# Kernel tuning notes

Hardware: AMD Instinct MI355X
Metric: run time of the kernel (lower is better)

Reference implementation:

```python
import jax, jax.numpy as jnp
import numpy as np

B, T, D, H, DH = 8, 1024, 512, 8, 64
DEPTH, V, FF = 8, 6400, 2048
NH, BS = 8, 64            # n_hashes, bucket_size
NB = T // BS              # 16 buckets
SELF_ATTN_VALUE = -5e4


def setup_inputs() -> dict:
    key = jax.random.key(0)
    ks = jax.random.split(key, 12)
    def n(k, shape, s=0.02):
        return jax.random.normal(k, shape, dtype=jnp.float32) * s
    return {
        "input_ids": jax.random.randint(ks[0], (B, T), 0, V),
        "token_emb": n(ks[1], (V, D)),
        "pos_emb": n(ks[2], (T, D)),
        "ln_attn_g": jnp.ones((DEPTH, D), jnp.float32),
        "ln_attn_b": jnp.zeros((DEPTH, D), jnp.float32),
        "Wqk": n(ks[3], (DEPTH, D, D)),
        "Wv": n(ks[4], (DEPTH, D, D)),
        "Wo": n(ks[5], (DEPTH, D, D)),
        "ln_ff_g": jnp.ones((DEPTH, D), jnp.float32),
        "ln_ff_b": jnp.zeros((DEPTH, D), jnp.float32),
        "W1": n(ks[6], (DEPTH, D, FF)),
        "b1": jnp.zeros((DEPTH, FF), jnp.float32),
        "W2": n(ks[7], (DEPTH, FF, D)),
        "b2": jnp.zeros((DEPTH, D), jnp.float32),
        "ln_f_g": jnp.ones((D,), jnp.float32),
        "ln_f_b": jnp.zeros((D,), jnp.float32),
        "Wfc": n(ks[8], (D, D)),
        # fixed random LSH rotation matrices, one per layer: [depth, dim_head, n_hashes, n_buckets//2]
        "rotations": jax.random.normal(ks[9], (DEPTH, DH, NH, NB // 2), dtype=jnp.float32),
    }


def layer_norm(x, g, b):
    m = jnp.mean(x, -1, keepdims=True)
    v = jnp.mean(jnp.square(x - m), -1, keepdims=True)
    return (x - m) * jax.lax.rsqrt(v + 1e-5) * g + b


def lsh_attention(x, Wqk, Wv, Wo, rot):
    """Reformer LSH self-attention: shared QK, NH hash rounds, bucket sort,
    chunked attention with 1-chunk look-back, multi-round logsumexp combine."""
    Bx = x.shape[0]
    qk = (x @ Wqk).reshape(Bx, T, H, DH).transpose(0, 2, 1, 3).reshape(Bx * H, T, DH)
    v = (x @ Wv).reshape(Bx, T, H, DH).transpose(0, 2, 1, 3).reshape(Bx * H, T, DH)

    # --- hashing: argmax over [rotated, -rotated] -> bucket ids per round ---
    rotated = jnp.einsum('btd,dhr->bhtr', qk, rot)                       # [BH,NH,T,NB/2]
    buckets = jnp.argmax(jnp.concatenate([rotated, -rotated], -1), -1)   # [BH,NH,T]
    buckets = buckets + (jnp.arange(NH) * NB)[None, :, None]
    buckets = buckets.reshape(Bx * H, NH * T)

    # --- stable sort by (bucket, position) ---
    ticker = jnp.arange(NH * T)
    b_t = buckets * T + (ticker % T)[None, :]
    sticker = jnp.argsort(b_t, axis=-1)
    undo = jnp.argsort(sticker, axis=-1)
    st = sticker % T                                                     # original positions
    sqk = jnp.take_along_axis(qk, st[..., None], axis=1)                 # [BH,NH*T,DH]
    sv = jnp.take_along_axis(v, st[..., None], axis=1)

    # --- chunk: NH*NB chunks of length BS, keys look back one chunk ---
    nc = NH * NB
    bq_t = st.reshape(-1, nc, BS)
    bq = sqk.reshape(-1, nc, BS, DH)
    bk = bq / (jnp.linalg.norm(bq, axis=-1, keepdims=True) + 1e-8)       # unit-length keys
    bv = sv.reshape(-1, nc, BS, DH)

    def look_back(t):
        return jnp.concatenate([t, jnp.roll(t, 1, axis=1)], axis=2)

    bk, bv, bkv_t = look_back(bk), look_back(bv), look_back(bq_t)

    dots = jnp.einsum('bnqd,bnkd->bnqk', bq, bk) * (DH ** -0.5)          # [BH,nc,BS,2BS]
    self_mask = bq_t[..., :, None] == bkv_t[..., None, :]
    dots = jnp.where(self_mask, SELF_ATTN_VALUE, dots)

    logits = jax.nn.logsumexp(dots, axis=-1, keepdims=True)
    probs = jnp.exp(dots - logits)
    bo = jnp.einsum('bnqk,bnkd->bnqd', probs, bv)

    # --- unsort and combine hash rounds weighted by per-round logsumexp ---
    so = bo.reshape(-1, NH * T, DH)
    slog = logits.reshape(-1, NH * T)
    o = jnp.take_along_axis(so, undo[..., None], axis=1).reshape(-1, NH, T, DH)
    lg = jnp.take_along_axis(slog, undo, axis=1).reshape(-1, NH, T, 1)
    w = jax.nn.softmax(lg, axis=1)
    out = jnp.sum(o * w, axis=1)                                         # [BH,T,DH]
    out = out.reshape(Bx, H, T, DH).transpose(0, 2, 1, 3).reshape(Bx, T, D)
    return out @ Wo


def reference(input_ids, token_emb, pos_emb, ln_attn_g, ln_attn_b, Wqk, Wv, Wo,
              ln_ff_g, ln_ff_b, W1, b1, W2, b2, ln_f_g, ln_f_b, Wfc, rotations):
    x = token_emb[input_ids] + pos_emb[None, :, :]
    # reversible residual streams: y1 = x1 + attn(norm(x2)); y2 = x2 + ff(norm(y1))
    x1, x2 = x, x
    for l in range(DEPTH):
        x1 = x1 + lsh_attention(layer_norm(x2, ln_attn_g[l], ln_attn_b[l]),
                                Wqk[l], Wv[l], Wo[l], rotations[l])
        h = layer_norm(x1, ln_ff_g[l], ln_ff_b[l])
        x2 = x2 + (jax.nn.gelu(h @ W1[l] + b1[l]) @ W2[l] + b2[l])
    x = 0.5 * (x1 + x2)
    x = layer_norm(x, ln_f_g, ln_f_b)
    return jnp.mean(x, axis=1) @ Wfc                                     # [B, embedding_dim]
```

## Files before the change

kernel.cpp:

```cpp
#include <hip/hip_runtime.h>
#include <hip/hip_bf16.h>
#include <cstdint>
#include <cstddef>

#define B_ 8
#define T_ 1024
#define D_ 512
#define H_ 8
#define DH_ 64
#define DEPTH_ 8
#define FF_ 2048
#define NH_ 8
#define BS_ 64
#define NB_ 16
#define NC_ 128
#define BH_ 64
#define ROWS_ 8192

typedef __attribute__((ext_vector_type(8))) short bf16x8;
typedef __attribute__((ext_vector_type(4))) float f32x4;

typedef __attribute__((address_space(1))) const unsigned int g_u32;
typedef __attribute__((address_space(3))) unsigned int l_u32;
__device__ __forceinline__ void gload16(const void* g, void* l) {
  __builtin_amdgcn_global_load_lds((g_u32*)g, (l_u32*)l, 16, 0, 0);
}

__device__ __forceinline__ float wave_sum(float v) {
#pragma unroll
  for (int o = 1; o < 64; o <<= 1) v += __shfl_xor(v, o);
  return v;
}

__device__ __forceinline__ float gelu_f(float u) {
  float c = u + 0.044715f * u * u * u;
  float t = tanhf(0.7978845608028654f * c);
  return 0.5f * u * (1.0f + t);
}

__global__ __launch_bounds__(128) void k_embed(const int* __restrict__ ids,
                                               const float* __restrict__ te,
                                               const float* __restrict__ pe,
                                               float* __restrict__ x1,
                                               float* __restrict__ x2) {
  int bt = blockIdx.x;
  int t = bt & (T_ - 1);
  int d = threadIdx.x * 4;
  int id = ids[bt];
  float4 v = *(const float4*)(te + (size_t)id * D_ + d);
  float4 p = *(const float4*)(pe + (size_t)t * D_ + d);
  v.x += p.x; v.y += p.y; v.z += p.z; v.w += p.w;
  *(float4*)(x1 + (size_t)bt * D_ + d) = v;
  *(float4*)(x2 + (size_t)bt * D_ + d) = v;
}

__global__ __launch_bounds__(256) void k_wt(const float* __restrict__ W,
                                            __hip_bfloat16* __restrict__ WT,
                                            int K, int N) {
  const float* Wl = W + (size_t)blockIdx.z * K * N;
  __hip_bfloat16* WTl = WT + (size_t)blockIdx.z * K * N;
  __shared__ float tile[32][33];
  int n0 = blockIdx.x * 32, k0 = blockIdx.y * 32;
  int tx = threadIdx.x & 31, ty = threadIdx.x >> 5;
#pragma unroll
  for (int i = 0; i < 32; i += 8)
    tile[ty + i][tx] = Wl[(size_t)(k0 + ty + i) * N + n0 + tx];
  __syncthreads();
#pragma unroll
  for (int i = 0; i < 32; i += 8)
    WTl[(size_t)(n0 + ty + i) * K + k0 + tx] = __float2bfloat16(tile[tx][ty + i]);
}

__global__ __launch_bounds__(256) void k_ln(const float* __restrict__ x,
                                            const float* __restrict__ xb,
                                            const float* __restrict__ g,
                                            const float* __restrict__ bb,
                                            float* __restrict__ y,
                                            __hip_bfloat16* __restrict__ yb) {
  int w = threadIdx.x >> 6, lane = threadIdx.x & 63;
  size_t row = (size_t)blockIdx.x * 4 + w;
  const float* xr = x + row * D_ + lane * 8;
  float v[8];
  *(float4*)(v)     = *(const float4*)(xr);
  *(float4*)(v + 4) = *(const float4*)(xr + 4);
  if (xb) {
    const float* x2r = xb + row * D_ + lane * 8;
    float u[8];
    *(float4*)(u)     = *(const float4*)(x2r);
    *(float4*)(u + 4) = *(const float4*)(x2r + 4);
#pragma unroll
    for (int i = 0; i < 8; ++i) v[i] = 0.5f * (v[i] + u[i]);
  }
  float s = 0.f;
#pragma unroll
  for (int i = 0; i < 8; ++i) s += v[i];
  s = wave_sum(s);
  float m = s * (1.0f / D_);
  float q = 0.f;
#pragma unroll
  for (int i = 0; i < 8; ++i) { float d = v[i] - m; q += d * d; }
  q = wave_sum(q);
  float inv = 1.0f / sqrtf(q * (1.0f / D_) + 1e-5f);
  float gg[8], bv[8];
  *(float4*)(gg)     = *(const float4*)(g + lane * 8);
  *(float4*)(gg + 4) = *(const float4*)(g + lane * 8 + 4);
  *(float4*)(bv)     = *(const float4*)(bb + lane * 8);
  *(float4*)(bv + 4) = *(const float4*)(bb + lane * 8 + 4);
  float o[8];
#pragma unroll
  for (int i = 0; i < 8; ++i) o[i] = (v[i] - m) * inv * gg[i] + bv[i];
  if (y) {
    float* yr = y + row * D_ + lane * 8;
    *(float4*)(yr)     = *(float4*)(o);
    *(float4*)(yr + 4) = *(float4*)(o + 4);
  }
  if (yb) {
    __hip_bfloat16 o16[8];
#pragma unroll
    for (int i = 0; i < 8; ++i) o16[i] = __float2bfloat16(o[i]);
    *(uint4*)(yb + row * D_ + lane * 8) = *(uint4*)o16;
  }
}

__global__ __launch_bounds__(256) void k_sgemm(const float* __restrict__ A,
                                               const float* __restrict__ Bm,
                                               float* __restrict__ C,
                                               int N, int K) {
  __shared__ float As[32][128];
  __shared__ float Bs[32][128];
  const int bn0 = blockIdx.x * 128;
  const int bm0 = blockIdx.y * 128;
  const int tid = threadIdx.x;
  const int w = tid >> 6, lane = tid & 63;
  const int wy = w >> 1, wx = w & 1;
  const int ly = lane >> 3, lx = lane & 7;
  const int rm = wy * 64 + ly * 8;
  const int cn = wx * 64 + lx * 8;
  float acc[8][8] = {};

  for (int k0 = 0; k0 < K; k0 += 32) {
#pragma unroll
    for (int ld = 0; ld < 4; ++ld) {
      int f = tid + ld * 256;
      int ar = f >> 3;
      int ac = (f & 7) << 2;
      float4 av = *(const float4*)(A + (size_t)(bm0 + ar) * K + k0 + ac);
      As[ac + 0][ar] = av.x; As[ac + 1][ar] = av.y;
      As[ac + 2][ar] = av.z; As[ac + 3][ar] = av.w;
      int br = f >> 5;
      int bc = (f & 31) << 2;
      *(float4*)(&Bs[br][bc]) = *(const float4*)(Bm + (size_t)(k0 + br) * N + bn0 + bc);
    }
    __syncthreads();
#pragma unroll
    for (int kk = 0; kk < 32; ++kk) {
      float a[8], b[8];
      *(float4*)(a)     = *(const float4*)(&As[kk][rm]);
      *(float4*)(a + 4) = *(const float4*)(&As[kk][rm + 4]);
      *(float4*)(b)     = *(const float4*)(&Bs[kk][cn]);
      *(float4*)(b + 4) = *(const float4*)(&Bs[kk][cn + 4]);
#pragma unroll
      for (int i = 0; i < 8; ++i)
#pragma unroll
        for (int j = 0; j < 8; ++j) acc[i][j] += a[i] * b[j];
    }
    __syncthreads();
  }
#pragma unroll
  for (int i = 0; i < 8; ++i) {
    float* crow = C + (size_t)(bm0 + rm + i) * N + bn0 + cn;
#pragma unroll
    for (int j0 = 0; j0 < 8; j0 += 4)
      *(float4*)(crow + j0) = make_float4(acc[i][j0], acc[i][j0 + 1], acc[i][j0 + 2], acc[i][j0 + 3]);
  }
}

template <int EPI>
__global__ __launch_bounds__(256) void k_bgemm(const __hip_bfloat16* __restrict__ A,
                                               const __hip_bfloat16* __restrict__ BT,
                                               const float* __restrict__ bias,
                                               void* __restrict__ Cv,
                                               int N, int K) {
  __shared__ __align__(16) __hip_bfloat16 As[128 * 32];
  __shared__ __align__(16) __hip_bfloat16 Bs[128 * 32];
  const int bn0 = blockIdx.x * 128;
  const int bm0 = blockIdx.y * 128;
  const int tid = threadIdx.x;
  const int w = tid >> 6, lane = tid & 63;
  const int wy = w >> 1, wx = w & 1;
  const int g = lane >> 4, lr = lane & 15;
  f32x4 acc[4][4] = {};

  const __hip_bfloat16* Abase = A + (size_t)bm0 * K;
  const __hip_bfloat16* Bbase = BT + (size_t)bn0 * K;

  for (int k0 = 0; k0 < K; k0 += 32) {
#pragma unroll
    for (int it = 0; it < 2; ++it) {
      int f = it * 256 + w * 64 + lane;
      int row = f >> 2;
      int kc = ((f & 3) ^ ((row >> 1) & 3)) << 3;
      gload16(Abase + (size_t)row * K + k0 + kc, &As[(it * 256 + w * 64) * 8]);
      gload16(Bbase + (size_t)row * K + k0 + kc, &Bs[(it * 256 + w * 64) * 8]);
    }
    __syncthreads();
    bf16x8 af[4], bfr[4];
#pragma unroll
    for (int m = 0; m < 4; ++m) {
      int row = wy * 64 + m * 16 + lr;
      af[m] = *(const bf16x8*)(&As[row * 32 + ((g ^ ((row >> 1) & 3)) << 3)]);
    }
#pragma unroll
    for (int n = 0; n < 4; ++n) {
      int row = wx * 64 + n * 16 + lr;
      bfr[n] = *(const bf16x8*)(&Bs[row * 32 + ((g ^ ((row >> 1) & 3)) << 3)]);
    }
#pragma unroll
    for (int m = 0; m < 4; ++m)
#pragma unroll
      for (int n = 0; n < 4; ++n)
        acc[m][n] = __builtin_amdgcn_mfma_f32_16x16x32_bf16(af[m], bfr[n], acc[m][n], 0, 0, 0);
    __syncthreads();
  }

  const int colb = bn0 + wx * 64 + lr;
  const int rowb = bm0 + wy * 64 + (g << 2);
#pragma unroll
  for (int m = 0; m < 4; ++m) {
#pragma unroll
    for (int n = 0; n < 4; ++n) {
      int c = colb + n * 16;
      int r0 = rowb + m * 16;
      float bsv = (EPI == 2 || EPI == 3) ? bias[c] : 0.f;
#pragma unroll
      for (int j = 0; j < 4; ++j) {
        float vlu = acc[m][n][j] + bsv;
        size_t idx = (size_t)(r0 + j) * N + c;
        if (EPI == 0) ((float*)Cv)[idx] = vlu;
        else if (EPI == 1) ((float*)Cv)[idx] += vlu;
        else if (EPI == 2) ((__hip_bfloat16*)Cv)[idx] = __float2bfloat16(gelu_f(vlu));
        else ((float*)Cv)[idx] += vlu;
      }
    }
  }
}

__global__ __launch_bounds__(128) void k_bucket(const float* __restrict__ qk,
                                                const float* __restrict__ rotL,
                                                unsigned char* __restrict__ bkt) {
  int blk = blockIdx.x;
  int tc = blk & 7, h = (blk >> 3) & 7, b = blk >> 6;
  int t0 = tc << 7;
  __shared__ float qs[128][65];
  __shared__ float rs[4096];
  int tid = threadIdx.x;
  for (int f = tid; f < 4096; f += 128) rs[f] = rotL[f];
  const float* base = qk + ((size_t)(b * T_ + t0)) * D_ + h * DH_;
  for (int f = tid; f < 2048; f += 128) {
    int rw = f >> 4, c4 = (f & 15) << 2;
    float4 v = *(const float4*)(base + (size_t)rw * D_ + c4);
    qs[rw][c4] = v.x; qs[rw][c4 + 1] = v.y; qs[rw][c4 + 2] = v.z; qs[rw][c4 + 3] = v.w;
  }
  __syncthreads();
  float s[64];
#pragma unroll
  for (int jr = 0; jr < 64; ++jr) s[jr] = 0.f;
  for (int d = 0; d < 64; ++d) {
    float q = qs[tid][d];
    const float* rp = rs + d * 64;
#pragma unroll
    for (int j4 = 0; j4 < 16; ++j4) {
      float4 rv = *(const float4*)(rp + j4 * 4);
      s[j4 * 4 + 0] += q * rv.x; s[j4 * 4 + 1] += q * rv.y;
      s[j4 * 4 + 2] += q * rv.z; s[j4 * 4 + 3] += q * rv.w;
    }
  }
  int bh = b * H_ + h;
#pragma unroll
  for (int r = 0; r < 8; ++r) {
    float best = s[r * 8];
    int bi = 0;
#pragma unroll
    for (int idx = 1; idx < 16; ++idx) {
      float v = (idx < 8) ? s[r * 8 + idx] : -s[r * 8 + idx - 8];
      if (v > best) { best = v; bi = idx; }
    }
    bkt[((size_t)(bh * NH_ + r)) * T_ + t0 + tid] = (unsigned char)bi;
  }
}

__global__ __launch_bounds__(1024) void k_sort(const unsigned char* __restrict__ bkt,
                                               int* __restrict__ st,
                                               int* __restrict__ undo) {
  int r = blockIdx.x & 7, bh = blockIdx.x >> 3;
  int t = threadIdx.x;
  int bk = bkt[((size_t)(bh * NH_ + r)) * T_ + t];
  int w = t >> 6, lane = t & 63;
  __shared__ int cnt[16][16];
  __shared__ int off[16][16];
  __shared__ int tot[16];
  __shared__ int stt[16];
  unsigned long long below = (1ULL << lane) - 1ULL;
  int myrank = 0;
#pragma unroll
  for (int bb = 0; bb < 16; ++bb) {
    unsigned long long m = __ballot(bk == bb);
    if (bk == bb) myrank = __popcll(m & below);
    if (lane == 0) cnt[w][bb] = __popcll(m);
  }
  __syncthreads();
  if (t < 16) {
    int run = 0;
    for (int ww = 0; ww < 16; ++ww) { off[ww][t] = run; run += cnt[ww][t]; }
    tot[t] = run;
  }
  __syncthreads();
  if (t == 0) {
    int run = 0;
    for (int bb = 0; bb < 16; ++bb) { stt[bb] = run; run += tot[bb]; }
  }
  __syncthreads();
  int pos = stt[bk] + off[w][bk] + myrank;
  st[((size_t)(bh * NH_ + r)) * T_ + pos] = t;
  undo[((size_t)(bh * NH_ + r)) * T_ + t] = pos;
}

__global__ __launch_bounds__(256) void k_attn(const float* __restrict__ qk,
                                              const float* __restrict__ vv,
                                              const int* __restrict__ st,
                                              __hip_bfloat16* __restrict__ ob,
                                              float* __restrict__ lgb) {
  __shared__ __align__(16) __hip_bfloat16 Kb[128 * 72];
  __shared__ __align__(16) __hip_bfloat16 VbT[64 * 136];
  __shared__ __align__(16) __hip_bfloat16 PbQb[64 * 136];
  __shared__ int pos[128];

  const int c = blockIdx.x, bh = blockIdx.y;
  const int b = bh >> 3, h = bh & 7;
  const int r = c >> 4;
  const int pc = (c + NC_ - 1) & (NC_ - 1);
  const int tid = threadIdx.x;

  if (tid < 128) {
    int sc = (tid < 64) ? c : pc;
    int slot = ((sc & 15) << 6) + (tid & 63);
    pos[tid] = st[((size_t)(bh * NH_ + (sc >> 4))) * T_ + slot];
  }
  __syncthreads();

  const float* qkbase = qk + ((size_t)b * T_) * D_ + h * DH_;
  const float* vbase  = vv + ((size_t)b * T_) * D_ + h * DH_;

#pragma unroll
  for (int ld = 0; ld < 8; ++ld) {
    int f = ld * 256 + tid;
    int rw = f >> 4, c4 = (f & 15) << 2;
    float4 v = *(const float4*)(qkbase + (size_t)pos[rw] * D_ + c4);
    float ss = v.x * v.x + v.y * v.y + v.z * v.z + v.w * v.w;
    ss += __shfl_xor(ss, 1); ss += __shfl_xor(ss, 2);
    ss += __shfl_xor(ss, 4); ss += __shfl_xor(ss, 8);
    float inv = 1.0f / (sqrtf(ss) + 1e-8f);
    __hip_bfloat16 kb4[4];
    kb4[0] = __float2bfloat16(v.x * inv); kb4[1] = __float2bfloat16(v.y * inv);
    kb4[2] = __float2bfloat16(v.z * inv); kb4[3] = __float2bfloat16(v.w * inv);
    *(uint2*)(&Kb[rw * 72 + c4]) = *(uint2*)kb4;
  }
#pragma unroll
  for (int ld = 0; ld < 4; ++ld) {
    int f = ld * 256 + tid;
    int rw = f >> 4, c4 = (f & 15) << 2;
    float4 v = *(const float4*)(qkbase + (size_t)pos[rw] * D_ + c4);
    __hip_bfloat16 qb4[4];
    qb4[0] = __float2bfloat16(v.x * 0.125f); qb4[1] = __float2bfloat16(v.y * 0.125f);
    qb4[2] = __float2bfloat16(v.z * 0.125f); qb4[3] = __float2bfloat16(v.w * 0.125f);
    *(uint2*)(&PbQb[rw * 72 + c4]) = *(uint2*)qb4;
  }
#pragma unroll
  for (int ld = 0; ld < 8; ++ld) {
    int f = ld * 256 + tid;
    int rw = f >> 4, c4 = (f & 15) << 2;
    float4 v = *(const float4*)(vbase + (size_t)pos[rw] * D_ + c4);
    VbT[(c4 + 0) * 136 + rw] = __float2bfloat16(v.x);
    VbT[(c4 + 1) * 136 + rw] = __float2bfloat16(v.y);
    VbT[(c4 + 2) * 136 + rw] = __float2bfloat16(v.z);
    VbT[(c4 + 3) * 136 + rw] = __float2bfloat16(v.w);
  }
  __syncthreads();

  const int w = tid >> 6, lane = tid & 63;
  const int g = lane >> 4, l15 = lane & 15;
  const int q0 = w * 16;

  bf16x8 af0 = *(const bf16x8*)(&PbQb[(q0 + l15) * 72 + g * 8]);
  bf16x8 af1 = *(const bf16x8*)(&PbQb[(q0 + l15) * 72 + 32 + g * 8]);
  f32x4 dacc[8];
#pragma unroll
  for (int n = 0; n < 8; ++n) dacc[n] = (f32x4){0.f, 0.f, 0.f, 0.f};
#pragma unroll
  for (int n = 0; n < 8; ++n) {
    bf16x8 b0 = *(const bf16x8*)(&Kb[(n * 16 + l15) * 72 + g * 8]);
    bf16x8 b1 = *(const bf16x8*)(&Kb[(n * 16 + l15) * 72 + 32 + g * 8]);
    dacc[n] = __builtin_amdgcn_mfma_f32_16x16x32_bf16(af0, b0, dacc[n], 0, 0, 0);
    dacc[n] = __builtin_amdgcn_mfma_f32_16x16x32_bf16(af1, b1, dacc[n], 0, 0, 0);
  }
  __syncthreads();

  int qpos[4], kpos[8];
#pragma unroll
  for (int reg = 0; reg < 4; ++reg) qpos[reg] = pos[q0 + g * 4 + reg];
#pragma unroll
  for (int n = 0; n < 8; ++n) kpos[n] = pos[n * 16 + l15];
  float pr[8][4];
  float lgt[4];
#pragma unroll
  for (int reg = 0; reg < 4; ++reg) {
    float mx = -3.0e38f;
#pragma unroll
    for (int n = 0; n < 8; ++n) {
      float dv = dacc[n][reg];
      dv = (kpos[n] == qpos[reg]) ? -5.0e4f : dv;
      pr[n][reg] = dv;
      mx = fmaxf(mx, dv);
    }
    mx = fmaxf(mx, __shfl_xor(mx, 1));
    mx = fmaxf(mx, __shfl_xor(mx, 2));
    mx = fmaxf(mx, __shfl_xor(mx, 4));
    mx = fmaxf(mx, __shfl_xor(mx, 8));
    float s = 0.f;
#pragma unroll
    for (int n = 0; n < 8; ++n) { float e = expf(pr[n][reg] - mx); pr[n][reg] = e; s += e; }
    s += __shfl_xor(s, 1); s += __shfl_xor(s, 2);
    s += __shfl_xor(s, 4); s += __shfl_xor(s, 8);
    lgt[reg] = mx + logf(s);
    float isc = 1.0f / s;
#pragma unroll
    for (int n = 0; n < 8; ++n) pr[n][reg] *= isc;
  }
#pragma unroll
  for (int n = 0; n < 8; ++n)
#pragma unroll
    for (int reg = 0; reg < 4; ++reg)
      PbQb[(q0 + g * 4 + reg) * 136 + n * 16 + l15] = __float2bfloat16(pr[n][reg]);
  const size_t slotbase = ((size_t)(bh * NH_ + r)) * T_ + ((c & 15) << 6);
  if (l15 == 0) {
#pragma unroll
    for (int reg = 0; reg < 4; ++reg)
      lgb[slotbase + q0 + g * 4 + reg] = lgt[reg];
  }
  __syncthreads();

  bf16x8 va[4];
#pragma unroll
  for (int s = 0; s < 4; ++s)
    va[s] = *(const bf16x8*)(&VbT[(w * 16 + l15) * 136 + s * 32 + g * 8]);
#pragma unroll
  for (int n = 0; n < 4; ++n) {
    f32x4 oa = (f32x4){0.f, 0.f, 0.f, 0.f};
#pragma unroll
    for (int s = 0; s < 4; ++s) {
      bf16x8 pb = *(const bf16x8*)(&PbQb[(n * 16 + l15) * 136 + s * 32 + g * 8]);
      oa = __builtin_amdgcn_mfma_f32_16x16x32_bf16(va[s], pb, oa, 0, 0, 0);
    }
    int q = n * 16 + l15;
    int d = w * 16 + g * 4;
    __hip_bfloat16 o4[4];
#pragma unroll
    for (int reg = 0; reg < 4; ++reg) o4[reg] = __float2bfloat16(oa[reg]);
    *(uint2*)(&ob[(slotbase + q) * DH_ + d]) = *(uint2*)o4;
  }
}

__global__ __launch_bounds__(256) void k_combine(const __hip_bfloat16* __restrict__ ob,
                                                 const float* __restrict__ lgb,
                                                 const int* __restrict__ undo,
                                                 __hip_bfloat16* __restrict__ attnb) {
  int g = threadIdx.x >> 6, lane = threadIdx.x & 63;
  int idx = blockIdx.x * 4 + g;
  int bh = idx >> 10, t = idx & (T_ - 1);
  int b = bh >> 3, h = bh & 7;
  int su[8];
  float lg[8];
  float m = -3.0e38f;
#pragma unroll
  for (int r = 0; r < 8; ++r) {
    su[r] = undo[((size_t)(bh * NH_ + r)) * T_ + t];
    lg[r] = lgb[((size_t)(bh * NH_ + r)) * T_ + su[r]];
    m = fmaxf(m, lg[r]);
  }
  float s = 0.f;
#pragma unroll
  for (int r = 0; r < 8; ++r) { lg[r] = expf(lg[r] - m); s += lg[r]; }
  float invs = 1.0f / s;
  float o = 0.f;
#pragma unroll
  for (int r = 0; r < 8; ++r)
    o += lg[r] * invs * __bfloat162float(ob[(((size_t)(bh * NH_ + r)) * T_ + su[r]) * DH_ + lane]);
  attnb[((size_t)(b * T_ + t)) * D_ + h * DH_ + lane] = __float2bfloat16(o);
}

__global__ void k_zero(float* __restrict__ p, int n) {
  int i = blockIdx.x * blockDim.x + threadIdx.x;
  if (i < n) p[i] = 0.f;
}

__global__ __launch_bounds__(256) void k_colsum(const float* __restrict__ xn,
                                                float* __restrict__ mean) {
  int b = blockIdx.x, dc = blockIdx.y, tc = blockIdx.z;
  int d = dc * 256 + threadIdx.x;
  float s = 0.f;
  for (int tt = 0; tt < 64; ++tt) {
    int t = tc * 64 + tt;
    s += xn[((size_t)(b * T_ + t)) * D_ + d];
  }
  atomicAdd(&mean[b * D_ + d], s);
}

__global__ __launch_bounds__(512) void k_fc(const float* __restrict__ mean,
                                            const float* __restrict__ Wfc,
                                            float* __restrict__ out) {
  int b = blockIdx.x, n = threadIdx.x;
  __shared__ float ms[512];
  ms[n] = mean[b * D_ + n] * (1.0f / 1024.0f);
  __syncthreads();
  float acc = 0.f;
  for (int d = 0; d < 512; ++d) acc += ms[d] * Wfc[(size_t)d * D_ + n];
  out[b * D_ + n] = acc;
}

extern "C" void kernel_launch(void* const* d_in, const int* in_sizes, int n_in,
                              void* d_out, int out_size, void* d_ws, size_t ws_size,
                              hipStream_t stream) {
  (void)in_sizes; (void)n_in; (void)out_size; (void)ws_size;
  const int*   ids  = (const int*)d_in[0];
  const float* te   = (const float*)d_in[1];
  const float* pe   = (const float*)d_in[2];
  const float* lag  = (const float*)d_in[3];
  const float* lab  = (const float*)d_in[4];
  const float* Wqk  = (const float*)d_in[5];
  const float* Wv   = (const float*)d_in[6];
  const float* Wo   = (const float*)d_in[7];
  const float* lfg  = (const float*)d_in[8];
  const float* lfb  = (const float*)d_in[9];
  const float* W1   = (const float*)d_in[10];
  const float* b1   = (const float*)d_in[11];
  const float* W2   = (const float*)d_in[12];
  const float* b2   = (const float*)d_in[13];
  const float* lnfg = (const float*)d_in[14];
  const float* lnfb = (const float*)d_in[15];
  const float* Wfc  = (const float*)d_in[16];
  const float* rot  = (const float*)d_in[17];

  char* ws = (char*)d_ws;
  size_t off = 0;
  auto carve = [&](size_t bytes) -> void* {
    void* p = ws + off;
    off += (bytes + 255) & ~(size_t)255;
    return p;
  };
  float* x1    = (float*)carve((size_t)ROWS_ * D_ * 4);
  float* x2    = (float*)carve((size_t)ROWS_ * D_ * 4);
  float* xn    = (float*)carve((size_t)ROWS_ * D_ * 4);
  float* qkb   = (float*)carve((size_t)ROWS_ * D_ * 4);
  float* vvb   = (float*)carve((size_t)ROWS_ * D_ * 4);
  __hip_bfloat16* xnb   = (__hip_bfloat16*)carve((size_t)ROWS_ * D_ * 2);
  __hip_bfloat16* attnb = (__hip_bfloat16*)carve((size_t)ROWS_ * D_ * 2);
  __hip_bfloat16* ob    = (__hip_bfloat16*)carve((size_t)BH_ * NH_ * T_ * DH_ * 2);
  __hip_bfloat16* hid   = ob;
  unsigned char* bkt = (unsigned char*)carve((size_t)BH_ * NH_ * T_);
  int*   stb   = (int*)carve((size_t)BH_ * NH_ * T_ * 4);
  int*   undo  = (int*)carve((size_t)BH_ * NH_ * T_ * 4);
  float* lgb   = (float*)carve((size_t)BH_ * NH_ * T_ * 4);
  float* meanb = (float*)carve((size_t)B_ * D_ * 4);
  __hip_bfloat16* WvT = (__hip_bfloat16*)carve((size_t)DEPTH_ * D_ * D_ * 2);
  __hip_bfloat16* WoT = (__hip_bfloat16*)carve((size_t)DEPTH_ * D_ * D_ * 2);
  __hip_bfloat16* W1T = (__hip_bfloat16*)carve((size_t)DEPTH_ * D_ * FF_ * 2);
  __hip_bfloat16* W2T = (__hip_bfloat16*)carve((size_t)DEPTH_ * FF_ * D_ * 2);

  k_wt<<<dim3(D_ / 32, D_ / 32, DEPTH_), 256, 0, stream>>>(Wv, WvT, D_, D_);
  k_wt<<<dim3(D_ / 32, D_ / 32, DEPTH_), 256, 0, stream>>>(Wo, WoT, D_, D_);
  k_wt<<<dim3(FF_ / 32, D_ / 32, DEPTH_), 256, 0, stream>>>(W1, W1T, D_, FF_);
  k_wt<<<dim3(D_ / 32, FF_ / 32, DEPTH_), 256, 0, stream>>>(W2, W2T, FF_, D_);

  k_embed<<<ROWS_, 128, 0, stream>>>(ids, te, pe, x1, x2);

  for (int l = 0; l < DEPTH_; ++l) {
    const float* wqk = Wqk + (size_t)l * D_ * D_;
    const __hip_bfloat16* wvt = WvT + (size_t)l * D_ * D_;
    const __hip_bfloat16* wot = WoT + (size_t)l * D_ * D_;
    const __hip_bfloat16* w1t = W1T + (size_t)l * D_ * FF_;
    const __hip_bfloat16* w2t = W2T + (size_t)l * FF_ * D_;

    k_ln<<<ROWS_ / 4, 256, 0, stream>>>(x2, nullptr, lag + l * D_, lab + l * D_, xn, xnb);
    k_sgemm<<<dim3(D_ / 128, ROWS_ / 128), 256, 0, stream>>>(xn, wqk, qkb, D_, D_);
    k_bgemm<0><<<dim3(D_ / 128, ROWS_ / 128), 256, 0, stream>>>(xnb, wvt, nullptr, vvb, D_, D_);
    k_bucket<<<512, 128, 0, stream>>>(qkb, rot + (size_t)l * 4096, bkt);
    k_sort<<<512, 1024, 0, stream>>>(bkt, stb, undo);
    k_attn<<<dim3(NC_, BH_), 256, 0, stream>>>(qkb, vvb, stb, ob, lgb);
    k_combine<<<BH_ * T_ / 4, 256, 0, stream>>>(ob, lgb, undo, attnb);
    k_bgemm<1><<<dim3(D_ / 128, ROWS_ / 128), 256, 0, stream>>>(attnb, wot, nullptr, x1, D_, D_);

    k_ln<<<ROWS_ / 4, 256, 0, stream>>>(x1, nullptr, lfg + l * D_, lfb + l * D_, nullptr, xnb);
    k_bgemm<2><<<dim3(FF_ / 128, ROWS_ / 128), 256, 0, stream>>>(xnb, w1t, b1 + l * FF_, hid, FF_, D_);
    k_bgemm<3><<<dim3(D_ / 128, ROWS_ / 128), 256, 0, stream>>>(hid, w2t, b2 + l * D_, x2, D_, FF_);
  }

  k_ln<<<ROWS_ / 4, 256, 0, stream>>>(x1, x2, lnfg, lnfb, xn, nullptr);
  k_zero<<<16, 256, 0, stream>>>(meanb, B_ * D_);
  k_colsum<<<dim3(B_, 2, 16), 256, 0, stream>>>(xn, meanb);
  k_fc<<<B_, 512, 0, stream>>>(meanb, Wfc, (float*)d_out);
}
```

Measured before the change: 3.312 ms.

## Precompute bf16 Q/normalized-K and bf16 V to shrink attention gathers

Adds a per-row prep kernel that writes scaled Q and L2-normalized K as bf16, and makes the V projection emit bf16. The attention kernel then gathers bf16 rows with 16-byte loads instead of fp32 rows, recomputing no norms. V is transposed into shared memory through lane shuffles, with an XOR swizzle to avoid bank conflicts. Softmax and combine switch to fast __expf/__logf. The cost is an extra kernel pass and extra bf16 buffers, plus reduced precision in the exp/log.

Measured after the change: 3.200 ms. 3.4% less time.

```diff
diff --git a/kernel.cpp b/kernel.cpp
--- a/kernel.cpp
+++ b/kernel.cpp
@@ -122,6 +122,30 @@
   }
 }
 
+__global__ __launch_bounds__(256) void k_prep(const float* __restrict__ qkb,
+                                              __hip_bfloat16* __restrict__ qsb,
+                                              __hip_bfloat16* __restrict__ knb) {
+  int w = threadIdx.x >> 6, lane = threadIdx.x & 63;
+  size_t row = (size_t)blockIdx.x * 4 + w;
+  const float* xr = qkb + row * D_ + lane * 8;
+  float v[8];
+  *(float4*)(v)     = *(const float4*)(xr);
+  *(float4*)(v + 4) = *(const float4*)(xr + 4);
+  float ss = 0.f;
+#pragma unroll
+  for (int i = 0; i < 8; ++i) ss += v[i] * v[i];
+  ss += __shfl_xor(ss, 1); ss += __shfl_xor(ss, 2); ss += __shfl_xor(ss, 4);
+  float inv = 1.0f / (sqrtf(ss) + 1e-8f);
+  __hip_bfloat16 qo[8], ko[8];
+#pragma unroll
+  for (int i = 0; i < 8; ++i) {
+    qo[i] = __float2bfloat16(v[i] * 0.125f);
+    ko[i] = __float2bfloat16(v[i] * inv);
+  }
+  *(uint4*)(qsb + row * D_ + lane * 8) = *(uint4*)qo;
+  *(uint4*)(knb + row * D_ + lane * 8) = *(uint4*)ko;
+}
+
 __global__ __launch_bounds__(256) void k_sgemm(const float* __restrict__ A,
                                                const float* __restrict__ Bm,
                                                float* __restrict__ C,
@@ -239,7 +263,8 @@
         if (EPI == 0) ((float*)Cv)[idx] = vlu;
         else if (EPI == 1) ((float*)Cv)[idx] += vlu;
         else if (EPI == 2) ((__hip_bfloat16*)Cv)[idx] = __float2bfloat16(gelu_f(vlu));
-        else ((float*)Cv)[idx] += vlu;
+        else if (EPI == 3) ((float*)Cv)[idx] += vlu;
+        else ((__hip_bfloat16*)Cv)[idx] = __float2bfloat16(vlu);
       }
     }
   }
@@ -325,8 +350,9 @@
   undo[((size_t)(bh * NH_ + r)) * T_ + t] = pos;
 }
 
-__global__ __launch_bounds__(256) void k_attn(const float* __restrict__ qk,
-                                              const float* __restrict__ vv,
+__global__ __launch_bounds__(256) void k_attn(const __hip_bfloat16* __restrict__ qs,
+                                              const __hip_bfloat16* __restrict__ kn,
+                                              const __hip_bfloat16* __restrict__ vv,
                                               const int* __restrict__ st,
                                               __hip_bfloat16* __restrict__ ob,
                                               float* __restrict__ lgb) {
@@ -348,42 +374,54 @@
   }
   __syncthreads();
 
-  const float* qkbase = qk + ((size_t)b * T_) * D_ + h * DH_;
-  const float* vbase  = vv + ((size_t)b * T_) * D_ + h * DH_;
-
-#pragma unroll
-  for (int ld = 0; ld < 8; ++ld) {
-    int f = ld * 256 + tid;
-    int rw = f >> 4, c4 = (f & 15) << 2;
-    float4 v = *(const float4*)(qkbase + (size_t)pos[rw] * D_ + c4);
-    float ss = v.x * v.x + v.y * v.y + v.z * v.z + v.w * v.w;
-    ss += __shfl_xor(ss, 1); ss += __shfl_xor(ss, 2);
-    ss += __shfl_xor(ss, 4); ss += __shfl_xor(ss, 8);
-    float inv = 1.0f / (sqrtf(ss) + 1e-8f);
-    __hip_bfloat16 kb4[4];
-    kb4[0] = __float2bfloat16(v.x * inv); kb4[1] = __float2bfloat16(v.y * inv);
-    kb4[2] = __float2bfloat16(v.z * inv); kb4[3] = __float2bfloat16(v.w * inv);
-    *(uint2*)(&Kb[rw * 72 + c4]) = *(uint2*)kb4;
-  }
+  const __hip_bfloat16* qbase = qs + ((size_t)b * T_) * D_ + h * DH_;
+  const __hip_bfloat16* kbase = kn + ((size_t)b * T_) * D_ + h * DH_;
+  const __hip_bfloat16* vbase = vv + ((size_t)b * T_) * D_ + h * DH_;
+
 #pragma unroll
   for (int ld = 0; ld < 4; ++ld) {
     int f = ld * 256 + tid;
-    int rw = f >> 4, c4 = (f & 15) << 2;
-    float4 v = *(const float4*)(qkbase + (size_t)pos[rw] * D_ + c4);
-    __hip_bfloat16 qb4[4];
-    qb4[0] = __float2bfloat16(v.x * 0.125f); qb4[1] = __float2bfloat16(v.y * 0.125f);
-    qb4[2] = __float2bfloat16(v.z * 0.125f); qb4[3] = __float2bfloat16(v.w * 0.125f);
-    *(uint2*)(&PbQb[rw * 72 + c4]) = *(uint2*)qb4;
-  }
-#pragma unroll
-  for (int ld = 0; ld < 8; ++ld) {
+    int rw = f >> 3, c8 = (f & 7) << 3;
+    *(uint4*)(&Kb[rw * 72 + c8]) = *(const uint4*)(kbase + (size_t)pos[rw] * D_ + c8);
+  }
+#pragma unroll
+  for (int ld = 0; ld < 2; ++ld) {
     int f = ld * 256 + tid;
-    int rw = f >> 4, c4 = (f & 15) << 2;
-    float4 v = *(const float4*)(vbase + (size_t)pos[rw] * D_ + c4);
-    VbT[(c4 + 0) * 136 + rw] = __float2bfloat16(v.x);
-    VbT[(c4 + 1) * 136 + rw] = __float2bfloat16(v.y);
-    VbT[(c4 + 2) * 136 + rw] = __float2bfloat16(v.z);
-    VbT[(c4 + 3) * 136 + rw] = __float2bfloat16(v.w);
+    int rw = f >> 3, c8 = (f & 7) << 3;
+    *(uint4*)(&PbQb[rw * 72 + c8]) = *(const uint4*)(qbase + (size_t)pos[rw] * D_ + c8);
+  }
+  {
+    const int w = tid >> 6, rl = tid & 7, d8 = (tid >> 3) & 7;
+#pragma unroll
+    for (int it = 0; it < 4; ++it) {
+      int rw0 = it * 32 + w * 8;
+      uint4 x = *(const uint4*)(vbase + (size_t)pos[rw0 + rl] * D_ + d8 * 8);
+      unsigned short u[8];
+      u[0] = x.x & 0xffff; u[1] = x.x >> 16;
+      u[2] = x.y & 0xffff; u[3] = x.y >> 16;
+      u[4] = x.z & 0xffff; u[5] = x.z >> 16;
+      u[6] = x.w & 0xffff; u[7] = x.w >> 16;
+#pragma unroll
+      for (int k = 0; k < 3; ++k) {
+        const int xm = 1 << k;
+        const bool sel = (rl >> k) & 1;
+#pragma unroll
+        for (int j0 = 0; j0 < 8; ++j0) {
+          if ((j0 >> k) & 1) continue;
+          int j1 = j0 | (1 << k);
+          unsigned int send = sel ? (unsigned int)u[j0] : (unsigned int)u[j1];
+          unsigned int recv = (unsigned int)__shfl_xor((int)send, xm);
+          if (sel) u[j0] = (unsigned short)recv; else u[j1] = (unsigned short)recv;
+        }
+      }
+      int d = d8 * 8 + rl;
+      uint4 y;
+      y.x = (unsigned int)u[0] | ((unsigned int)u[1] << 16);
+      y.y = (unsigned int)u[2] | ((unsigned int)u[3] << 16);
+      y.z = (unsigned int)u[4] | ((unsigned int)u[5] << 16);
+      y.w = (unsigned int)u[6] | ((unsigned int)u[7] << 16);
+      *(uint4*)(&VbT[d * 136 + (rw0 ^ (((d >> 3) & 3) << 3))]) = y;
+    }
   }
   __syncthreads();
 
@@ -428,10 +466,10 @@
     mx = fmaxf(mx, __shfl_xor(mx, 8));
     float s = 0.f;
 #pragma unroll
-    for (int n = 0; n < 8; ++n) { float e = expf(pr[n][reg] - mx); pr[n][reg] = e; s += e; }
+    for (int n = 0; n < 8; ++n) { float e = __expf(pr[n][reg] - mx); pr[n][reg] = e; s += e; }
     s += __shfl_xor(s, 1); s += __shfl_xor(s, 2);
     s += __shfl_xor(s, 4); s += __shfl_xor(s, 8);
-    lgt[reg] = mx + logf(s);
+    lgt[reg] = mx + __logf(s);
     float isc = 1.0f / s;
 #pragma unroll
     for (int n = 0; n < 8; ++n) pr[n][reg] *= isc;
@@ -451,8 +489,10 @@
 
   bf16x8 va[4];
 #pragma unroll
-  for (int s = 0; s < 4; ++s)
-    va[s] = *(const bf16x8*)(&VbT[(w * 16 + l15) * 136 + s * 32 + g * 8]);
+  for (int s = 0; s < 4; ++s) {
+    int dd = w * 16 + l15;
+    va[s] = *(const bf16x8*)(&VbT[dd * 136 + ((s * 32 + g * 8) ^ (((dd >> 3) & 3) << 3))]);
+  }
 #pragma unroll
   for (int n = 0; n < 4; ++n) {
     f32x4 oa = (f32x4){0.f, 0.f, 0.f, 0.f};
@@ -489,7 +529,7 @@
   }
   float s = 0.f;
 #pragma unroll
-  for (int r = 0; r < 8; ++r) { lg[r] = expf(lg[r] - m); s += lg[r]; }
+  for (int r = 0; r < 8; ++r) { lg[r] = __expf(lg[r] - m); s += lg[r]; }
   float invs = 1.0f / s;
   float o = 0.f;
 #pragma unroll
@@ -561,7 +601,9 @@
   float* x2    = (float*)carve((size_t)ROWS_ * D_ * 4);
   float* xn    = (float*)carve((size_t)ROWS_ * D_ * 4);
   float* qkb   = (float*)carve((size_t)ROWS_ * D_ * 4);
-  float* vvb   = (float*)carve((size_t)ROWS_ * D_ * 4);
+  __hip_bfloat16* vvb   = (__hip_bfloat16*)carve((size_t)ROWS_ * D_ * 2);
+  __hip_bfloat16* qsb   = (__hip_bfloat16*)carve((size_t)ROWS_ * D_ * 2);
+  __hip_bfloat16* knb   = (__hip_bfloat16*)carve((size_t)ROWS_ * D_ * 2);
   __hip_bfloat16* xnb   = (__hip_bfloat16*)carve((size_t)ROWS_ * D_ * 2);
   __hip_bfloat16* attnb = (__hip_bfloat16*)carve((size_t)ROWS_ * D_ * 2);
   __hip_bfloat16* ob    = (__hip_bfloat16*)carve((size_t)BH_ * NH_ * T_ * DH_ * 2);
@@ -592,10 +634,11 @@
 
     k_ln<<<ROWS_ / 4, 256, 0, stream>>>(x2, nullptr, lag + l * D_, lab + l * D_, xn, xnb);
     k_sgemm<<<dim3(D_ / 128, ROWS_ / 128), 256, 0, stream>>>(xn, wqk, qkb, D_, D_);
-    k_bgemm<0><<<dim3(D_ / 128, ROWS_ / 128), 256, 0, stream>>>(xnb, wvt, nullptr, vvb, D_, D_);
+    k_bgemm<4><<<dim3(D_ / 128, ROWS_ / 128), 256, 0, stream>>>(xnb, wvt, nullptr, vvb, D_, D_);
+    k_prep<<<ROWS_ / 4, 256, 0, stream>>>(qkb, qsb, knb);
     k_bucket<<<512, 128, 0, stream>>>(qkb, rot + (size_t)l * 4096, bkt);
     k_sort<<<512, 1024, 0, stream>>>(bkt, stb, undo);
-    k_attn<<<dim3(NC_, BH_), 256, 0, stream>>>(qkb, vvb, stb, ob, lgb);
+    k_attn<<<dim3(NC_, BH_), 256, 0, stream>>>(qsb, knb, vvb, stb, ob, lgb);
     k_combine<<<BH_ * T_ / 4, 256, 0, stream>>>(ob, lgb, undo, attnb);
     k_bgemm<1><<<dim3(D_ / 128, ROWS_ / 128), 256, 0, stream>>>(attnb, wot, nullptr, x1, D_, D_);
 
```
